# Kernel tuning notes

Hardware: AMD Instinct MI355X
Metric: run time of the kernel (lower is better)

## Reference

```python
import jax, jax.numpy as jnp
import numpy as np

D_MODEL = 512
HIDDEN_MULT = 4
D_FF = D_MODEL * HIDDEN_MULT
B, L = 4, 1024


def setup_inputs() -> dict:
    key = jax.random.key(0)
    ks = jax.random.split(key, 7)
    s1 = 1.0 / np.sqrt(D_MODEL)
    s2 = 1.0 / np.sqrt(D_FF)
    return {
        "x": jax.random.normal(ks[0], (B, L, D_MODEL), dtype=jnp.float32),
        "W1": jax.random.uniform(ks[1], (D_FF, D_MODEL), minval=-s1, maxval=s1, dtype=jnp.float32),
        "b1": jax.random.uniform(ks[2], (D_FF,), minval=-s1, maxval=s1, dtype=jnp.float32),
        "W2": jax.random.uniform(ks[3], (D_MODEL, D_FF), minval=-s2, maxval=s2, dtype=jnp.float32),
        "b2": jax.random.uniform(ks[4], (D_MODEL,), minval=-s2, maxval=s2, dtype=jnp.float32),
        "Lambda_raw_F": jax.random.uniform(ks[5], (D_FF, D_MODEL), minval=-3.0, maxval=3.0, dtype=jnp.float32),
        "Gamma_F": jax.random.uniform(ks[6], (D_FF, D_MODEL), minval=-0.5 * s1, maxval=0.5 * s1, dtype=jnp.float32),
    }


def _stp_forward(x, W1, b1, W2, b2, Lambda_raw_F, Gamma_F):
    # x: (B, L, D)
    retention = 1.0 - jax.nn.sigmoid(Lambda_raw_F)  # (d_ff, D)
    gamma = Gamma_F
    # static contribution of W1: (B, L, d_ff)
    static_h = jnp.einsum('bld,fd->blf', x, W1) + b1

    def step(F_state, inputs):
        # F_state: (B, d_ff, D); x_t: (B, D); sh_t: (B, d_ff)
        x_t, sh_t = inputs
        h_pre = sh_t + jnp.einsum('bfd,bd->bf', F_state, x_t)
        h = jax.nn.gelu(h_pre, approximate=False)
        out = jnp.einsum('bf,df->bd', h, W2) + b2
        # Hebbian outer-product update
        F_new = retention[None] * F_state + gamma[None] * (h_pre[:, :, None] * x_t[:, None, :])
        return F_new, out

    F0 = jnp.zeros((x.shape[0], W1.shape[0], W1.shape[1]), dtype=x.dtype)
    xs = (jnp.swapaxes(x, 0, 1), jnp.swapaxes(static_h, 0, 1))  # (L, B, ...)
    _, ys = jax.lax.scan(step, F0, xs)
    return jnp.swapaxes(ys, 0, 1)  # (B, L, D)


def reference(x, W1, b1, W2, b2, Lambda_raw_F, Gamma_F):
    return _stp_forward(x, W1, b1, W2, b2, Lambda_raw_F, Gamma_F)
```

## Files before the change

### kernel.cpp

```cpp
#include <hip/hip_runtime.h>
#include <cstdint>

#define DM   512
#define DFF  2048
#define BSZ  4
#define LSEQ 1024

__device__ __forceinline__ float4 f4fma(float4 a, float4 b, float4 c) {
    return make_float4(fmaf(a.x, b.x, c.x), fmaf(a.y, b.y, c.y),
                       fmaf(a.z, b.z, c.z), fmaf(a.w, b.w, c.w));
}
__device__ __forceinline__ float4 f4mul(float4 a, float4 b) {
    return make_float4(a.x * b.x, a.y * b.y, a.z * b.z, a.w * b.w);
}

__global__ __launch_bounds__(256, 2)
void stp_scan(const float* __restrict__ x,
              const float* __restrict__ W1,
              const float* __restrict__ b1,
              const float* __restrict__ Lam,
              const float* __restrict__ Gam,
              float* __restrict__ hbuf)
{
    const int tid  = threadIdx.x;
    const int lane = tid & 63;
    const int w    = tid >> 6;
    const int j    = lane & 15;
    const int g    = lane >> 4;
    const int b    = blockIdx.x >> 7;
    const int fbase = (blockIdx.x & 127) << 4;
    const int f    = fbase + w * 4 + g;

    __shared__ float4 xs[2][128];

    const float4* __restrict__ x4 =
        reinterpret_cast<const float4*>(x + (size_t)b * LSEQ * DM);

    float4 FW[8], R[8], G[8], WR[8];
    {
        const float4* lr = reinterpret_cast<const float4*>(Lam + (size_t)f * DM);
        const float4* gr = reinterpret_cast<const float4*>(Gam + (size_t)f * DM);
        const float4* wr = reinterpret_cast<const float4*>(W1  + (size_t)f * DM);
        #pragma unroll
        for (int k = 0; k < 8; ++k) {
            const int idx = j + 16 * k;
            float4 lv = lr[idx];
            float4 rv;
            rv.x = 1.0f / (1.0f + expf(lv.x));
            rv.y = 1.0f / (1.0f + expf(lv.y));
            rv.z = 1.0f / (1.0f + expf(lv.z));
            rv.w = 1.0f / (1.0f + expf(lv.w));
            R[k] = rv;
            G[k] = gr[idx];
            float4 wv = wr[idx];
            FW[k] = wv;
            WR[k].x = wv.x * (1.0f - rv.x);
            WR[k].y = wv.y * (1.0f - rv.y);
            WR[k].z = wv.z * (1.0f - rv.z);
            WR[k].w = wv.w * (1.0f - rv.w);
        }
    }
    const float b1v = b1[f];

    if (tid < 128) xs[0][tid] = x4[tid];
    __syncthreads();

    float* __restrict__ hout = hbuf + (size_t)b * LSEQ * DFF + f;

    #pragma unroll 1
    for (int t = 0; t < LSEQ; ++t) {
        const int cur = t & 1;

        float4 stage;
        const bool do_stage = ((t + 1) < LSEQ) && (tid < 128);
        if (do_stage) stage = x4[(t + 1) * 128 + tid];

        float4 xr[8];
        #pragma unroll
        for (int k = 0; k < 8; ++k) xr[k] = xs[cur][j + 16 * k];

        float4 a0 = make_float4(0.f, 0.f, 0.f, 0.f);
        float4 a1 = make_float4(0.f, 0.f, 0.f, 0.f);
        #pragma unroll
        for (int k = 0; k < 8; k += 2) {
            a0 = f4fma(FW[k],     xr[k],     a0);
            a1 = f4fma(FW[k + 1], xr[k + 1], a1);
        }
        float p = (a0.x + a1.x) + (a0.y + a1.y) + (a0.z + a1.z) + (a0.w + a1.w);

        p += __shfl_xor(p, 1);
        p += __shfl_xor(p, 2);
        p += __shfl_xor(p, 4);
        p += __shfl_xor(p, 8);

        const float hp = p + b1v;

        const float hg = 0.5f * hp * (1.0f + erff(hp * 0.70710678118654752f));

        #pragma unroll
        for (int k = 0; k < 8; ++k) {
            float4 gx = f4mul(G[k], xr[k]);
            float4 s;
            s.x = fmaf(gx.x, hp, WR[k].x);
            s.y = fmaf(gx.y, hp, WR[k].y);
            s.z = fmaf(gx.z, hp, WR[k].z);
            s.w = fmaf(gx.w, hp, WR[k].w);
            FW[k] = f4fma(R[k], FW[k], s);
        }

        if (j == 0) hout[(size_t)t * DFF] = hg;

        if (do_stage) xs[cur ^ 1][tid] = stage;
        __syncthreads();
    }
}

__global__ __launch_bounds__(256)
void gemm_nt_bias(const float* __restrict__ A,
                  const float* __restrict__ Bm,
                  const float* __restrict__ bias,
                  float* __restrict__ C,
                  int M, int N, int K)
{
    __shared__ float As[16][68];
    __shared__ float Bs[16][68];

    const int tid = threadIdx.x;
    const int tx  = tid & 15;
    const int ty  = tid >> 4;
    const int row0 = blockIdx.y * 64;
    const int col0 = blockIdx.x * 64;

    const int lr = tid >> 2;
    const int lk = (tid & 3) << 2;

    const float* Aptr = A  + (size_t)(row0 + lr) * K + lk;
    const float* Bptr = Bm + (size_t)(col0 + lr) * K + lk;

    float acc[4][4] = {};
    float4 av = *reinterpret_cast<const float4*>(Aptr);
    float4 bv = *reinterpret_cast<const float4*>(Bptr);

    const int NT = K >> 4;
    for (int kt = 0; kt < NT; ++kt) {
        __syncthreads();
        As[lk + 0][lr] = av.x; As[lk + 1][lr] = av.y;
        As[lk + 2][lr] = av.z; As[lk + 3][lr] = av.w;
        Bs[lk + 0][lr] = bv.x; Bs[lk + 1][lr] = bv.y;
        Bs[lk + 2][lr] = bv.z; Bs[lk + 3][lr] = bv.w;
        __syncthreads();

        if (kt + 1 < NT) {
            av = *reinterpret_cast<const float4*>(Aptr + (kt + 1) * 16);
            bv = *reinterpret_cast<const float4*>(Bptr + (kt + 1) * 16);
        }

        #pragma unroll
        for (int k = 0; k < 16; ++k) {
            float4 a = *reinterpret_cast<const float4*>(&As[k][ty * 4]);
            float4 bb = *reinterpret_cast<const float4*>(&Bs[k][tx * 4]);
            acc[0][0] = fmaf(a.x, bb.x, acc[0][0]);
            acc[0][1] = fmaf(a.x, bb.y, acc[0][1]);
            acc[0][2] = fmaf(a.x, bb.z, acc[0][2]);
            acc[0][3] = fmaf(a.x, bb.w, acc[0][3]);
            acc[1][0] = fmaf(a.y, bb.x, acc[1][0]);
            acc[1][1] = fmaf(a.y, bb.y, acc[1][1]);
            acc[1][2] = fmaf(a.y, bb.z, acc[1][2]);
            acc[1][3] = fmaf(a.y, bb.w, acc[1][3]);
            acc[2][0] = fmaf(a.z, bb.x, acc[2][0]);
            acc[2][1] = fmaf(a.z, bb.y, acc[2][1]);
            acc[2][2] = fmaf(a.z, bb.z, acc[2][2]);
            acc[2][3] = fmaf(a.z, bb.w, acc[2][3]);
            acc[3][0] = fmaf(a.w, bb.x, acc[3][0]);
            acc[3][1] = fmaf(a.w, bb.y, acc[3][1]);
            acc[3][2] = fmaf(a.w, bb.z, acc[3][2]);
            acc[3][3] = fmaf(a.w, bb.w, acc[3][3]);
        }
    }

    const float4 bb = *reinterpret_cast<const float4*>(&bias[col0 + tx * 4]);
    #pragma unroll
    for (int i = 0; i < 4; ++i) {
        float4 o;
        o.x = acc[i][0] + bb.x;
        o.y = acc[i][1] + bb.y;
        o.z = acc[i][2] + bb.z;
        o.w = acc[i][3] + bb.w;
        *reinterpret_cast<float4*>(&C[(size_t)(row0 + ty * 4 + i) * N + col0 + tx * 4]) = o;
    }
}

extern "C" void kernel_launch(void* const* d_in, const int* in_sizes, int n_in,
                              void* d_out, int out_size, void* d_ws, size_t ws_size,
                              hipStream_t stream)
{
    const float* x   = (const float*)d_in[0];
    const float* W1  = (const float*)d_in[1];
    const float* b1  = (const float*)d_in[2];
    const float* W2  = (const float*)d_in[3];
    const float* b2  = (const float*)d_in[4];
    const float* Lam = (const float*)d_in[5];
    const float* Gam = (const float*)d_in[6];
    float* out  = (float*)d_out;
    float* hbuf = (float*)d_ws;

    stp_scan<<<dim3(BSZ * (DFF / 16)), dim3(256), 0, stream>>>(x, W1, b1, Lam, Gam, hbuf);

    dim3 g2(DM / 64, (BSZ * LSEQ) / 64);
    gemm_nt_bias<<<g2, dim3(256), 0, stream>>>(hbuf, W2, b2, out, BSZ * LSEQ, DM, DFF);
}
```

Baseline: 757.9 us.

## Spread scan rows over 32 lanes and drop shared-memory staging and barriers

The scan kernel now gives each feature row to 32 lanes instead of 16, which halves the per-thread register state and doubles the grid to 1024 blocks. Occupancy hint rises to 4 blocks per CU. The shared-memory double buffer and the per-step __syncthreads are gone: each thread loads its own slice of the next x vector straight from global memory (L1/L2 cached) and prefetches it one step ahead in registers. The goal is to remove barrier stalls and raise parallelism on the latency-bound recurrence, at the cost of redundant global loads of x and one extra shuffle step per reduction.

```diff
diff --git a/kernel.cpp b/kernel.cpp
--- a/kernel.cpp
+++ b/kernel.cpp
@@ -14,7 +14,7 @@
     return make_float4(a.x * b.x, a.y * b.y, a.z * b.z, a.w * b.w);
 }
 
-__global__ __launch_bounds__(256, 2)
+__global__ __launch_bounds__(256, 4)
 void stp_scan(const float* __restrict__ x,
               const float* __restrict__ W1,
               const float* __restrict__ b1,
@@ -24,26 +24,24 @@
 {
     const int tid  = threadIdx.x;
     const int lane = tid & 63;
-    const int w    = tid >> 6;
-    const int j    = lane & 15;
-    const int g    = lane >> 4;
-    const int b    = blockIdx.x >> 7;
-    const int fbase = (blockIdx.x & 127) << 4;
-    const int f    = fbase + w * 4 + g;
-
-    __shared__ float4 xs[2][128];
+    const int wid  = tid >> 6;
+    const int j    = lane & 31;
+    const int g    = lane >> 5;
+    const int b    = blockIdx.x >> 8;
+    const int fbase = (blockIdx.x & 255) << 3;
+    const int f    = fbase + (wid << 1) + g;
 
     const float4* __restrict__ x4 =
         reinterpret_cast<const float4*>(x + (size_t)b * LSEQ * DM);
 
-    float4 FW[8], R[8], G[8], WR[8];
+    float4 FW[4], R[4], G[4], WR[4];
     {
         const float4* lr = reinterpret_cast<const float4*>(Lam + (size_t)f * DM);
         const float4* gr = reinterpret_cast<const float4*>(Gam + (size_t)f * DM);
         const float4* wr = reinterpret_cast<const float4*>(W1  + (size_t)f * DM);
         #pragma unroll
-        for (int k = 0; k < 8; ++k) {
-            const int idx = j + 16 * k;
+        for (int k = 0; k < 4; ++k) {
+            const int idx = j + 32 * k;
             float4 lv = lr[idx];
             float4 rv;
             rv.x = 1.0f / (1.0f + expf(lv.x));
@@ -62,43 +60,37 @@
     }
     const float b1v = b1[f];
 
-    if (tid < 128) xs[0][tid] = x4[tid];
-    __syncthreads();
-
     float* __restrict__ hout = hbuf + (size_t)b * LSEQ * DFF + f;
 
-    #pragma unroll 1
+    float4 xr[4];
+    #pragma unroll
+    for (int k = 0; k < 4; ++k) xr[k] = x4[j + 32 * k];
+
+    #pragma unroll 2
     for (int t = 0; t < LSEQ; ++t) {
-        const int cur = t & 1;
-
-        float4 stage;
-        const bool do_stage = ((t + 1) < LSEQ) && (tid < 128);
-        if (do_stage) stage = x4[(t + 1) * 128 + tid];
-
-        float4 xr[8];
-        #pragma unroll
-        for (int k = 0; k < 8; ++k) xr[k] = xs[cur][j + 16 * k];
-
-        float4 a0 = make_float4(0.f, 0.f, 0.f, 0.f);
-        float4 a1 = make_float4(0.f, 0.f, 0.f, 0.f);
-        #pragma unroll
-        for (int k = 0; k < 8; k += 2) {
-            a0 = f4fma(FW[k],     xr[k],     a0);
-            a1 = f4fma(FW[k + 1], xr[k + 1], a1);
-        }
-        float p = (a0.x + a1.x) + (a0.y + a1.y) + (a0.z + a1.z) + (a0.w + a1.w);
+        const int tn = (t + 1 < LSEQ) ? (t + 1) : t;
+        float4 xn[4];
+        #pragma unroll
+        for (int k = 0; k < 4; ++k) xn[k] = x4[tn * 128 + j + 32 * k];
+
+        float4 acc = make_float4(0.f, 0.f, 0.f, 0.f);
+        #pragma unroll
+        for (int k = 0; k < 4; ++k) acc = f4fma(FW[k], xr[k], acc);
+        float p = (acc.x + acc.y) + (acc.z + acc.w);
 
         p += __shfl_xor(p, 1);
         p += __shfl_xor(p, 2);
         p += __shfl_xor(p, 4);
         p += __shfl_xor(p, 8);
+        p += __shfl_xor(p, 16);
 
         const float hp = p + b1v;
 
         const float hg = 0.5f * hp * (1.0f + erff(hp * 0.70710678118654752f));
-
-        #pragma unroll
-        for (int k = 0; k < 8; ++k) {
+        if (j == 0) hout[(size_t)t * DFF] = hg;
+
+        #pragma unroll
+        for (int k = 0; k < 4; ++k) {
             float4 gx = f4mul(G[k], xr[k]);
             float4 s;
             s.x = fmaf(gx.x, hp, WR[k].x);
@@ -108,10 +100,8 @@
             FW[k] = f4fma(R[k], FW[k], s);
         }
 
-        if (j == 0) hout[(size_t)t * DFF] = hg;
-
-        if (do_stage) xs[cur ^ 1][tid] = stage;
-        __syncthreads();
+        #pragma unroll
+        for (int k = 0; k < 4; ++k) xr[k] = xn[k];
     }
 }
 
@@ -204,7 +194,7 @@
     float* out  = (float*)d_out;
     float* hbuf = (float*)d_ws;
 
-    stp_scan<<<dim3(BSZ * (DFF / 16)), dim3(256), 0, stream>>>(x, W1, b1, Lam, Gam, hbuf);
+    stp_scan<<<dim3(BSZ * (DFF / 8)), dim3(256), 0, stream>>>(x, W1, b1, Lam, Gam, hbuf);
 
     dim3 g2(DM / 64, (BSZ * LSEQ) / 64);
     gemm_nt_bias<<<g2, dim3(256), 0, stream>>>(hbuf, W2, b2, out, BSZ * LSEQ, DM, DFF);
```

Result: slower. 915.2 us (+20.8%).
